# Kernel optimization log

Measured on AMD Instinct MI355X. Metric: run time of the kernel, lower is better.

## Reference

```python
import jax, jax.numpy as jnp
import numpy as np

B, TQ, TV, D, U = 4, 256, 256, 512, 128
NEG = -1e9  # Keras masked-softmax large negative


def setup_inputs() -> dict:
    key = jax.random.key(0)
    kq, kv, km, k1, k2, ks = jax.random.split(key, 6)
    query = jax.random.normal(kq, (B, TQ, D), dtype=jnp.float32)
    value = jax.random.normal(kv, (B, TV, D), dtype=jnp.float32)
    mask = jax.random.uniform(km, (B, TV)) < 0.9  # bool value mask, mostly valid
    # Dense(units, use_bias=False) weights, glorot-style scaling
    W1 = jax.random.normal(k1, (D, U), dtype=jnp.float32) * (2.0 / (D + U)) ** 0.5
    W2 = jax.random.normal(k2, (D, U), dtype=jnp.float32) * (2.0 / (D + U)) ** 0.5
    # AdditiveAttention use_scale=True learned scale vector [units]
    scale = jax.random.normal(ks, (U,), dtype=jnp.float32) * 0.1
    return {"query": query, "value": value, "mask": mask,
            "W1": W1, "W2": W2, "scale": scale}


def reference(query, value, mask, W1, W2, scale):
    # Dense projections (no bias)
    q = jnp.einsum("bqd,du->bqu", query, W1)   # [B,Tq,U]
    k = jnp.einsum("bvd,du->bvu", value, W2)   # [B,Tv,U]
    # Bahdanau additive scores: sum_u scale_u * tanh(q + k) -> [B,Tq,Tv]
    scores = jnp.einsum("u,bqvu->bqv", scale,
                        jnp.tanh(q[:, :, None, :] + k[:, None, :, :]))
    # masked softmax over the value axis
    scores = jnp.where(mask[:, None, :], scores, NEG)
    weights = jax.nn.softmax(scores, axis=-1)  # [B,Tq,Tv]
    # weighted sum of (unprojected) values; query_mask is all-ones -> no-op
    context = jnp.einsum("bqv,bvd->bqd", weights, value)  # [B,Tq,D]
    return context, weights
```

## Files before the change

kernel.cpp:

```cpp
#include <hip/hip_runtime.h>
#include <math.h>

#define BB 4
#define TQ 256
#define TV 256
#define DD 512
#define UU 128
#define NEGV (-1e9f)

__device__ __forceinline__ float fast_rcp(float x) {
    return __builtin_amdgcn_rcpf(x);
}

__global__ __launch_bounds__(512, 4) void proj_kernel(
    const float* __restrict__ query, const float* __restrict__ value,
    const float* __restrict__ W1, const float* __restrict__ W2,
    float* __restrict__ eqp ,
    float* __restrict__ ekT ) {
    int bid = blockIdx.x;
    int which = bid >> 8;
    int row0 = (bid & 255) * 4;
    const float* X = which ? value : query;
    const float* W = which ? W2 : W1;

    __shared__ float xs[4 * DD];
    __shared__ float cmb[3][4][UU];
    int tid = threadIdx.x;
    ((float4*)xs)[tid] = ((const float4*)(X + (size_t)row0 * DD))[tid];
    __syncthreads();

    int kc = tid >> 7;
    int u = tid & 127;
    const float* Wp = W + (size_t)(kc * (DD / 4)) * UU + u;
    const float* x0 = xs + kc * (DD / 4);
    float a0 = 0.f, a1 = 0.f, a2 = 0.f, a3 = 0.f;
    #pragma unroll 8
    for (int d = 0; d < DD / 4; ++d) {
        float w = Wp[(size_t)d * UU];
        a0 = fmaf(x0[d], w, a0);
        a1 = fmaf(x0[DD + d], w, a1);
        a2 = fmaf(x0[2 * DD + d], w, a2);
        a3 = fmaf(x0[3 * DD + d], w, a3);
    }
    if (kc) {
        cmb[kc - 1][0][u] = a0; cmb[kc - 1][1][u] = a1;
        cmb[kc - 1][2][u] = a2; cmb[kc - 1][3][u] = a3;
    }
    __syncthreads();
    if (!kc) {
        a0 = __expf(2.f * (((a0 + cmb[0][0][u]) + cmb[1][0][u]) + cmb[2][0][u]));
        a1 = __expf(2.f * (((a1 + cmb[0][1][u]) + cmb[1][1][u]) + cmb[2][1][u]));
        a2 = __expf(2.f * (((a2 + cmb[0][2][u]) + cmb[1][2][u]) + cmb[2][2][u]));
        a3 = __expf(2.f * (((a3 + cmb[0][3][u]) + cmb[1][3][u]) + cmb[2][3][u]));
        if (which == 0) {
            float* p = eqp + (size_t)row0 * UU + u;
            p[0 * UU] = a0; p[1 * UU] = a1; p[2 * UU] = a2; p[3 * UU] = a3;
        } else {
            int b = row0 >> 8, v0 = row0 & 255;
            float* p = ekT + ((size_t)b * UU + u) * TV + v0;
            p[0] = a0; p[1] = a1; p[2] = a2; p[3] = a3;
        }
    }
}

__global__ __launch_bounds__(1024, 4) void attn_kernel(
    const float* __restrict__ eqp, const float* __restrict__ ekT,
    const float* __restrict__ scale, const unsigned char* __restrict__ m,
    const float* __restrict__ value,
    float* __restrict__ ctx, float* __restrict__ weights) {
    int blk = blockIdx.x;
    int b = blk >> 6;
    int q0 = (blk & 63) * 4;
    int tid = threadIdx.x;

    __shared__ float eq4[4][UU];
    __shared__ float sc2[UU];
    __shared__ union {
        float pb[7][4][TV];
        float2 part[3][4][256];
    } un;
    __shared__ float sv[4][TV];
    __shared__ float redM[4][4], redS[4][4];
    __shared__ int flagF, flagB;

    if (tid == 0) { flagF = 0; flagB = 0; }
    if (tid < 512) eq4[tid >> 7][tid & 127] = eqp[(size_t)(b * TQ + q0) * UU + tid];
    else if (tid < 512 + UU) sc2[tid - 512] = -2.f * scale[tid - 512];
    if (tid < 256) {
        uchar4 c4 = ((const uchar4*)m)[tid];
        if (c4.w == 0x3f) flagF = 1;
        if (c4.y | c4.z | c4.w) flagB = 1;
    }
    __syncthreads();

    {
        int vp = tid & 127;
        int h = tid >> 7;
        const float2* kb2 = (const float2*)(ekT + ((size_t)b * UU + h * 16) * TV) + vp;
        const float* eqh0 = &eq4[0][h * 16];
        const float* eqh1 = &eq4[1][h * 16];
        const float* eqh2 = &eq4[2][h * 16];
        const float* eqh3 = &eq4[3][h * 16];
        const float* sch = &sc2[h * 16];
        float ax0 = 0.f, ax1 = 0.f, ax2 = 0.f, ax3 = 0.f;
        float ay0 = 0.f, ay1 = 0.f, ay2 = 0.f, ay3 = 0.f;
        #pragma unroll
        for (int i = 0; i < 16; ++i) {
            float2 ek = kb2[(size_t)i * (TV / 2)];
            float w2 = sch[i];
            float e0 = eqh0[i], e1 = eqh1[i], e2 = eqh2[i], e3 = eqh3[i];
            ax0 = fmaf(w2, fast_rcp(fmaf(e0, ek.x, 1.f)), ax0);
            ay0 = fmaf(w2, fast_rcp(fmaf(e0, ek.y, 1.f)), ay0);
            ax1 = fmaf(w2, fast_rcp(fmaf(e1, ek.x, 1.f)), ax1);
            ay1 = fmaf(w2, fast_rcp(fmaf(e1, ek.y, 1.f)), ay1);
            ax2 = fmaf(w2, fast_rcp(fmaf(e2, ek.x, 1.f)), ax2);
            ay2 = fmaf(w2, fast_rcp(fmaf(e2, ek.y, 1.f)), ay2);
            ax3 = fmaf(w2, fast_rcp(fmaf(e3, ek.x, 1.f)), ax3);
            ay3 = fmaf(w2, fast_rcp(fmaf(e3, ek.y, 1.f)), ay3);
        }
        if (h > 0) {
            un.pb[h - 1][0][2 * vp] = ax0; un.pb[h - 1][0][2 * vp + 1] = ay0;
            un.pb[h - 1][1][2 * vp] = ax1; un.pb[h - 1][1][2 * vp + 1] = ay1;
            un.pb[h - 1][2][2 * vp] = ax2; un.pb[h - 1][2][2 * vp + 1] = ay2;
            un.pb[h - 1][3][2 * vp] = ax3; un.pb[h - 1][3][2 * vp + 1] = ay3;
        }
        __syncthreads();
        if (h == 0) {
            float rx0 = ax0, ry0 = ay0, rx1 = ax1, ry1 = ay1;
            float rx2 = ax2, ry2 = ay2, rx3 = ax3, ry3 = ay3;
            #pragma unroll
            for (int j = 0; j < 7; ++j) {
                rx0 += un.pb[j][0][2 * vp]; ry0 += un.pb[j][0][2 * vp + 1];
                rx1 += un.pb[j][1][2 * vp]; ry1 += un.pb[j][1][2 * vp + 1];
                rx2 += un.pb[j][2][2 * vp]; ry2 += un.pb[j][2][2 * vp + 1];
                rx3 += un.pb[j][3][2 * vp]; ry3 += un.pb[j][3][2 * vp + 1];
            }
            sv[0][2 * vp] = rx0; sv[0][2 * vp + 1] = ry0;
            sv[1][2 * vp] = rx1; sv[1][2 * vp + 1] = ry1;
            sv[2][2 * vp] = rx2; sv[2][2 * vp + 1] = ry2;
            sv[3][2 * vp] = rx3; sv[3][2 * vp + 1] = ry3;
        }
        __syncthreads();
    }

    {
        int v = tid & 255;
        float mk;
        {
            int idx = b * TV + v;
            bool ok;
            if (flagF)      ok = (m[4 * idx + 3] != 0);
            else if (flagB) ok = (m[idx] != 0);
            else            ok = (m[4 * idx] != 0);
            mk = ok ? __builtin_inff() : NEGV;
        }
        float s[4], e[4];
        #pragma unroll
        for (int r = 0; r < 4; ++r) s[r] = fminf(sv[r][v], mk);

        int wid = tid >> 6, lane = tid & 63;
        #pragma unroll
        for (int r = 0; r < 4; ++r) {
            float mm = s[r];
            #pragma unroll
            for (int off = 32; off >= 1; off >>= 1) mm = fmaxf(mm, __shfl_xor(mm, off));
            if (tid < 256 && lane == 0) redM[r][wid] = mm;
        }
        __syncthreads();
        #pragma unroll
        for (int r = 0; r < 4; ++r) {
            float mfull = fmaxf(fmaxf(redM[r][0], redM[r][1]),
                                fmaxf(redM[r][2], redM[r][3]));
            e[r] = __expf(s[r] - mfull);
            float t = e[r];
            #pragma unroll
            for (int off = 32; off >= 1; off >>= 1) t += __shfl_xor(t, off);
            if (tid < 256 && lane == 0) redS[r][wid] = t;
        }
        __syncthreads();
        if (tid < 256) {
            #pragma unroll
            for (int r = 0; r < 4; ++r) {
                float rs = fast_rcp((redS[r][0] + redS[r][1]) + (redS[r][2] + redS[r][3]));
                float wv = e[r] * rs;
                weights[(size_t)(b * TQ + q0 + r) * TV + v] = wv;
                sv[r][v] = wv;
            }
        }
        __syncthreads();
    }

    {
        int dp = tid & 255;
        int vh = tid >> 8;
        const float2* vb = (const float2*)(value + ((size_t)b * TV + vh * 64) * DD) + dp;
        const float* wr0 = &sv[0][vh * 64];
        const float* wr1 = &sv[1][vh * 64];
        const float* wr2 = &sv[2][vh * 64];
        const float* wr3 = &sv[3][vh * 64];
        float cx0 = 0.f, cx1 = 0.f, cx2 = 0.f, cx3 = 0.f;
        float cy0 = 0.f, cy1 = 0.f, cy2 = 0.f, cy3 = 0.f;
        #pragma unroll 16
        for (int t = 0; t < 64; ++t) {
            float2 vv = vb[(size_t)t * (DD / 2)];
            float w0 = wr0[t], w1 = wr1[t], w2 = wr2[t], w3 = wr3[t];
            cx0 = fmaf(w0, vv.x, cx0); cy0 = fmaf(w0, vv.y, cy0);
            cx1 = fmaf(w1, vv.x, cx1); cy1 = fmaf(w1, vv.y, cy1);
            cx2 = fmaf(w2, vv.x, cx2); cy2 = fmaf(w2, vv.y, cy2);
            cx3 = fmaf(w3, vv.x, cx3); cy3 = fmaf(w3, vv.y, cy3);
        }
        if (vh > 0) {
            un.part[vh - 1][0][dp] = make_float2(cx0, cy0);
            un.part[vh - 1][1][dp] = make_float2(cx1, cy1);
            un.part[vh - 1][2][dp] = make_float2(cx2, cy2);
            un.part[vh - 1][3][dp] = make_float2(cx3, cy3);
        }
        __syncthreads();
        if (vh == 0) {
            float2 o0 = make_float2(cx0 + un.part[0][0][dp].x + un.part[1][0][dp].x + un.part[2][0][dp].x,
                                    cy0 + un.part[0][0][dp].y + un.part[1][0][dp].y + un.part[2][0][dp].y);
            float2 o1 = make_float2(cx1 + un.part[0][1][dp].x + un.part[1][1][dp].x + un.part[2][1][dp].x,
                                    cy1 + un.part[0][1][dp].y + un.part[1][1][dp].y + un.part[2][1][dp].y);
            float2 o2 = make_float2(cx2 + un.part[0][2][dp].x + un.part[1][2][dp].x + un.part[2][2][dp].x,
                                    cy2 + un.part[0][2][dp].y + un.part[1][2][dp].y + un.part[2][2][dp].y);
            float2 o3 = make_float2(cx3 + un.part[0][3][dp].x + un.part[1][3][dp].x + un.part[2][3][dp].x,
                                    cy3 + un.part[0][3][dp].y + un.part[1][3][dp].y + un.part[2][3][dp].y);
            ((float2*)(ctx + (size_t)(b * TQ + q0 + 0) * DD))[dp] = o0;
            ((float2*)(ctx + (size_t)(b * TQ + q0 + 1) * DD))[dp] = o1;
            ((float2*)(ctx + (size_t)(b * TQ + q0 + 2) * DD))[dp] = o2;
            ((float2*)(ctx + (size_t)(b * TQ + q0 + 3) * DD))[dp] = o3;
        }
    }
}

extern "C" void kernel_launch(void* const* d_in, const int* in_sizes, int n_in,
                              void* d_out, int out_size, void* d_ws, size_t ws_size,
                              hipStream_t stream) {
    const float* query = (const float*)d_in[0];
    const float* value = (const float*)d_in[1];
    const unsigned char* mask = (const unsigned char*)d_in[2];
    const float* W1 = (const float*)d_in[3];
    const float* W2 = (const float*)d_in[4];
    const float* scale = (const float*)d_in[5];

    float* ctx = (float*)d_out;
    float* weights = (float*)d_out + (size_t)BB * TQ * DD;

    float* eqp = (float*)d_ws;
    float* ekT = eqp + (size_t)BB * TQ * UU;

    proj_kernel<<<512, 512, 0, stream>>>(query, value, W1, W2, eqp, ekT);
    attn_kernel<<<256, 1024, 0, stream>>>(eqp, ekT, scale, mask, value, ctx, weights);
}
```

Before: 29.93 us.

## Split attention into 512 blocks of 2 query rows with float4 context loads

```diff
diff --git a/kernel.cpp b/kernel.cpp
--- a/kernel.cpp
+++ b/kernel.cpp
@@ -63,29 +63,27 @@
     }
 }
 
-__global__ __launch_bounds__(1024, 4) void attn_kernel(
+__global__ __launch_bounds__(512, 4) void attn_kernel(
     const float* __restrict__ eqp, const float* __restrict__ ekT,
     const float* __restrict__ scale, const unsigned char* __restrict__ m,
     const float* __restrict__ value,
     float* __restrict__ ctx, float* __restrict__ weights) {
     int blk = blockIdx.x;
-    int b = blk >> 6;
-    int q0 = (blk & 63) * 4;
+    int b = blk >> 7;
+    int q0 = (blk & 127) * 2;
     int tid = threadIdx.x;
 
-    __shared__ float eq4[4][UU];
+    __shared__ float eq2[2][UU];
     __shared__ float sc2[UU];
-    __shared__ union {
-        float pb[7][4][TV];
-        float2 part[3][4][256];
-    } un;
-    __shared__ float sv[4][TV];
-    __shared__ float redM[4][4], redS[4][4];
+    __shared__ float pb[3][2][TV];
+    __shared__ float4 part4[3][2][128];
+    __shared__ float sv[2][TV];
+    __shared__ float redM[2][4], redS[2][4];
     __shared__ int flagF, flagB;
 
     if (tid == 0) { flagF = 0; flagB = 0; }
-    if (tid < 512) eq4[tid >> 7][tid & 127] = eqp[(size_t)(b * TQ + q0) * UU + tid];
-    else if (tid < 512 + UU) sc2[tid - 512] = -2.f * scale[tid - 512];
+    if (tid < 2 * UU) eq2[tid >> 7][tid & 127] = eqp[(size_t)(b * TQ + q0) * UU + tid];
+    else if (tid < 3 * UU) sc2[tid - 2 * UU] = -2.f * scale[tid - 2 * UU];
     if (tid < 256) {
         uchar4 c4 = ((const uchar4*)m)[tid];
         if (c4.w == 0x3f) flagF = 1;
@@ -96,49 +94,35 @@
     {
         int vp = tid & 127;
         int h = tid >> 7;
-        const float2* kb2 = (const float2*)(ekT + ((size_t)b * UU + h * 16) * TV) + vp;
-        const float* eqh0 = &eq4[0][h * 16];
-        const float* eqh1 = &eq4[1][h * 16];
-        const float* eqh2 = &eq4[2][h * 16];
-        const float* eqh3 = &eq4[3][h * 16];
-        const float* sch = &sc2[h * 16];
-        float ax0 = 0.f, ax1 = 0.f, ax2 = 0.f, ax3 = 0.f;
-        float ay0 = 0.f, ay1 = 0.f, ay2 = 0.f, ay3 = 0.f;
-        #pragma unroll
-        for (int i = 0; i < 16; ++i) {
+        const float2* kb2 = (const float2*)(ekT + ((size_t)b * UU + h * 32) * TV) + vp;
+        const float* eqh0 = &eq2[0][h * 32];
+        const float* eqh1 = &eq2[1][h * 32];
+        const float* sch = &sc2[h * 32];
+        float ax0 = 0.f, ay0 = 0.f, ax1 = 0.f, ay1 = 0.f;
+        #pragma unroll
+        for (int i = 0; i < 32; ++i) {
             float2 ek = kb2[(size_t)i * (TV / 2)];
             float w2 = sch[i];
-            float e0 = eqh0[i], e1 = eqh1[i], e2 = eqh2[i], e3 = eqh3[i];
+            float e0 = eqh0[i], e1 = eqh1[i];
             ax0 = fmaf(w2, fast_rcp(fmaf(e0, ek.x, 1.f)), ax0);
             ay0 = fmaf(w2, fast_rcp(fmaf(e0, ek.y, 1.f)), ay0);
             ax1 = fmaf(w2, fast_rcp(fmaf(e1, ek.x, 1.f)), ax1);
             ay1 = fmaf(w2, fast_rcp(fmaf(e1, ek.y, 1.f)), ay1);
-            ax2 = fmaf(w2, fast_rcp(fmaf(e2, ek.x, 1.f)), ax2);
-            ay2 = fmaf(w2, fast_rcp(fmaf(e2, ek.y, 1.f)), ay2);
-            ax3 = fmaf(w2, fast_rcp(fmaf(e3, ek.x, 1.f)), ax3);
-            ay3 = fmaf(w2, fast_rcp(fmaf(e3, ek.y, 1.f)), ay3);
         }
         if (h > 0) {
-            un.pb[h - 1][0][2 * vp] = ax0; un.pb[h - 1][0][2 * vp + 1] = ay0;
-            un.pb[h - 1][1][2 * vp] = ax1; un.pb[h - 1][1][2 * vp + 1] = ay1;
-            un.pb[h - 1][2][2 * vp] = ax2; un.pb[h - 1][2][2 * vp + 1] = ay2;
-            un.pb[h - 1][3][2 * vp] = ax3; un.pb[h - 1][3][2 * vp + 1] = ay3;
+            pb[h - 1][0][2 * vp] = ax0; pb[h - 1][0][2 * vp + 1] = ay0;
+            pb[h - 1][1][2 * vp] = ax1; pb[h - 1][1][2 * vp + 1] = ay1;
         }
         __syncthreads();
         if (h == 0) {
             float rx0 = ax0, ry0 = ay0, rx1 = ax1, ry1 = ay1;
-            float rx2 = ax2, ry2 = ay2, rx3 = ax3, ry3 = ay3;
-            #pragma unroll
-            for (int j = 0; j < 7; ++j) {
-                rx0 += un.pb[j][0][2 * vp]; ry0 += un.pb[j][0][2 * vp + 1];
-                rx1 += un.pb[j][1][2 * vp]; ry1 += un.pb[j][1][2 * vp + 1];
-                rx2 += un.pb[j][2][2 * vp]; ry2 += un.pb[j][2][2 * vp + 1];
-                rx3 += un.pb[j][3][2 * vp]; ry3 += un.pb[j][3][2 * vp + 1];
+            #pragma unroll
+            for (int j = 0; j < 3; ++j) {
+                rx0 += pb[j][0][2 * vp]; ry0 += pb[j][0][2 * vp + 1];
+                rx1 += pb[j][1][2 * vp]; ry1 += pb[j][1][2 * vp + 1];
             }
             sv[0][2 * vp] = rx0; sv[0][2 * vp + 1] = ry0;
             sv[1][2 * vp] = rx1; sv[1][2 * vp + 1] = ry1;
-            sv[2][2 * vp] = rx2; sv[2][2 * vp + 1] = ry2;
-            sv[3][2 * vp] = rx3; sv[3][2 * vp + 1] = ry3;
         }
         __syncthreads();
     }
@@ -154,13 +138,13 @@
             else            ok = (m[4 * idx] != 0);
             mk = ok ? __builtin_inff() : NEGV;
         }
-        float s[4], e[4];
-        #pragma unroll
-        for (int r = 0; r < 4; ++r) s[r] = fminf(sv[r][v], mk);
+        float s[2], e[2];
+        #pragma unroll
+        for (int r = 0; r < 2; ++r) s[r] = fminf(sv[r][v], mk);
 
         int wid = tid >> 6, lane = tid & 63;
         #pragma unroll
-        for (int r = 0; r < 4; ++r) {
+        for (int r = 0; r < 2; ++r) {
             float mm = s[r];
             #pragma unroll
             for (int off = 32; off >= 1; off >>= 1) mm = fmaxf(mm, __shfl_xor(mm, off));
@@ -168,7 +152,7 @@
         }
         __syncthreads();
         #pragma unroll
-        for (int r = 0; r < 4; ++r) {
+        for (int r = 0; r < 2; ++r) {
             float mfull = fmaxf(fmaxf(redM[r][0], redM[r][1]),
                                 fmaxf(redM[r][2], redM[r][3]));
             e[r] = __expf(s[r] - mfull);
@@ -180,7 +164,7 @@
         __syncthreads();
         if (tid < 256) {
             #pragma unroll
-            for (int r = 0; r < 4; ++r) {
+            for (int r = 0; r < 2; ++r) {
                 float rs = fast_rcp((redS[r][0] + redS[r][1]) + (redS[r][2] + redS[r][3]));
                 float wv = e[r] * rs;
                 weights[(size_t)(b * TQ + q0 + r) * TV + v] = wv;
@@ -191,44 +175,36 @@
     }
 
     {
-        int dp = tid & 255;
-        int vh = tid >> 8;
-        const float2* vb = (const float2*)(value + ((size_t)b * TV + vh * 64) * DD) + dp;
+        int df = tid & 127;
+        int vh = tid >> 7;
+        const float4* vb = (const float4*)(value + ((size_t)b * TV + vh * 64) * DD) + df;
         const float* wr0 = &sv[0][vh * 64];
         const float* wr1 = &sv[1][vh * 64];
-        const float* wr2 = &sv[2][vh * 64];
-        const float* wr3 = &sv[3][vh * 64];
-        float cx0 = 0.f, cx1 = 0.f, cx2 = 0.f, cx3 = 0.f;
-        float cy0 = 0.f, cy1 = 0.f, cy2 = 0.f, cy3 = 0.f;
+        float4 c0 = make_float4(0.f, 0.f, 0.f, 0.f);
+        float4 c1 = make_float4(0.f, 0.f, 0.f, 0.f);
         #pragma unroll 16
         for (int t = 0; t < 64; ++t) {
-            float2 vv = vb[(size_t)t * (DD / 2)];
-            float w0 = wr0[t], w1 = wr1[t], w2 = wr2[t], w3 = wr3[t];
-            cx0 = fmaf(w0, vv.x, cx0); cy0 = fmaf(w0, vv.y, cy0);
-            cx1 = fmaf(w1, vv.x, cx1); cy1 = fmaf(w1, vv.y, cy1);
-            cx2 = fmaf(w2, vv.x, cx2); cy2 = fmaf(w2, vv.y, cy2);
-            cx3 = fmaf(w3, vv.x, cx3); cy3 = fmaf(w3, vv.y, cy3);
+            float4 vv = vb[(size_t)t * (DD / 4)];
+            float w0 = wr0[t], w1 = wr1[t];
+            c0.x = fmaf(w0, vv.x, c0.x); c0.y = fmaf(w0, vv.y, c0.y);
+            c0.z = fmaf(w0, vv.z, c0.z); c0.w = fmaf(w0, vv.w, c0.w);
+            c1.x = fmaf(w1, vv.x, c1.x); c1.y = fmaf(w1, vv.y, c1.y);
+            c1.z = fmaf(w1, vv.z, c1.z); c1.w = fmaf(w1, vv.w, c1.w);
         }
         if (vh > 0) {
-            un.part[vh - 1][0][dp] = make_float2(cx0, cy0);
-            un.part[vh - 1][1][dp] = make_float2(cx1, cy1);
-            un.part[vh - 1][2][dp] = make_float2(cx2, cy2);
-            un.part[vh - 1][3][dp] = make_float2(cx3, cy3);
+            part4[vh - 1][0][df] = c0;
+            part4[vh - 1][1][df] = c1;
         }
         __syncthreads();
         if (vh == 0) {
-            float2 o0 = make_float2(cx0 + un.part[0][0][dp].x + un.part[1][0][dp].x + un.part[2][0][dp].x,
-                                    cy0 + un.part[0][0][dp].y + un.part[1][0][dp].y + un.part[2][0][dp].y);
-            float2 o1 = make_float2(cx1 + un.part[0][1][dp].x + un.part[1][1][dp].x + un.part[2][1][dp].x,
-                                    cy1 + un.part[0][1][dp].y + un.part[1][1][dp].y + un.part[2][1][dp].y);
-            float2 o2 = make_float2(cx2 + un.part[0][2][dp].x + un.part[1][2][dp].x + un.part[2][2][dp].x,
-                                    cy2 + un.part[0][2][dp].y + un.part[1][2][dp].y + un.part[2][2][dp].y);
-            float2 o3 = make_float2(cx3 + un.part[0][3][dp].x + un.part[1][3][dp].x + un.part[2][3][dp].x,
-                                    cy3 + un.part[0][3][dp].y + un.part[1][3][dp].y + un.part[2][3][dp].y);
-            ((float2*)(ctx + (size_t)(b * TQ + q0 + 0) * DD))[dp] = o0;
-            ((float2*)(ctx + (size_t)(b * TQ + q0 + 1) * DD))[dp] = o1;
-            ((float2*)(ctx + (size_t)(b * TQ + q0 + 2) * DD))[dp] = o2;
-            ((float2*)(ctx + (size_t)(b * TQ + q0 + 3) * DD))[dp] = o3;
+            #pragma unroll
+            for (int j = 0; j < 3; ++j) {
+                float4 p0 = part4[j][0][df], p1 = part4[j][1][df];
+                c0.x += p0.x; c0.y += p0.y; c0.z += p0.z; c0.w += p0.w;
+                c1.x += p1.x; c1.y += p1.y; c1.z += p1.z; c1.w += p1.w;
+            }
+            ((float4*)(ctx + (size_t)(b * TQ + q0 + 0) * DD))[df] = c0;
+            ((float4*)(ctx + (size_t)(b * TQ + q0 + 1) * DD))[df] = c1;
         }
     }
 }
@@ -250,5 +226,5 @@
     float* ekT = eqp + (size_t)BB * TQ * UU;
 
     proj_kernel<<<512, 512, 0, stream>>>(query, value, W1, W2, eqp, ekT);
-    attn_kernel<<<256, 1024, 0, stream>>>(eqp, ekT, scale, mask, value, ctx, weights);
-}
+    attn_kernel<<<512, 512, 0, stream>>>(eqp, ekT, scale, mask, value, ctx, weights);
+}
```

New measurement: 32.34 us. +8.1%, slower.
